# Kernel tuning notes

Hardware: AMD Instinct MI355X
Metric: run time of the kernel (lower is better)

Reference implementation:

```python
import jax, jax.numpy as jnp
import numpy as np

K = 3; PAD = 1; CIN = 64; COUT = 64; B = 4; H = 128; W = 128


def setup_inputs() -> dict:
    key = jax.random.key(0)
    k1, k2, k3 = jax.random.split(key, 3)
    x = jax.random.normal(k1, (B, CIN, H, W), dtype=jnp.float32)
    # offset-predicting conv: [2*K*K, Cin, K, K]; small init -> sub-pixel offsets
    w_off = jax.random.normal(k2, (2 * K * K, CIN, K, K), dtype=jnp.float32) * 0.01
    b_off = jnp.zeros((2 * K * K,), dtype=jnp.float32)
    # deformable conv weight (bias=False): [Cout, Cin, K, K]
    w_def = jax.random.normal(k3, (COUT, CIN, K, K), dtype=jnp.float32) * 0.05
    return {"x": x, "w_off": w_off, "b_off": b_off, "w_def": w_def}


def _deform_conv(x, w_off, b_off, w_def):
    Bb, Cin, Hh, Ww = x.shape
    KK = K * K
    # 1) predict offsets with a regular 3x3 conv (stride 1, pad 1)
    off = jax.lax.conv_general_dilated(
        x, w_off, window_strides=(1, 1), padding=[(PAD, PAD), (PAD, PAD)],
        dimension_numbers=("NCHW", "OIHW", "NCHW"))
    off = off + b_off[None, :, None, None]          # [B, 2*KK, H, W]
    off = off.reshape(Bb, KK, 2, Hh, Ww)            # torchvision layout: (dy, dx) per tap
    dy, dx = off[:, :, 0], off[:, :, 1]             # [B, KK, H, W]

    # 2) sampling coordinates: p = p0 + p_k + offset
    ky = (jnp.arange(KK) // K).astype(x.dtype)
    kx = (jnp.arange(KK) % K).astype(x.dtype)
    hh = jnp.arange(Hh, dtype=x.dtype)
    ww = jnp.arange(Ww, dtype=x.dtype)
    py = hh[None, None, :, None] - PAD + ky[None, :, None, None] + dy   # [B,KK,H,W]
    px = ww[None, None, None, :] - PAD + kx[None, :, None, None] + dx

    # 3) bilinear sampling with zero padding outside the image
    y0f = jnp.floor(py); x0f = jnp.floor(px)
    fy = py - y0f; fx = px - x0f
    y0 = y0f.astype(jnp.int32); x0 = x0f.astype(jnp.int32)
    x_flat = x.reshape(Bb, Cin, Hh * Ww)

    def gather(yi, xi):
        valid = (yi >= 0) & (yi < Hh) & (xi >= 0) & (xi < Ww)
        idx = jnp.clip(yi, 0, Hh - 1) * Ww + jnp.clip(xi, 0, Ww - 1)     # [B,KK,H,W]
        g = jax.vmap(lambda xf, ix: xf[:, ix.reshape(-1)])(x_flat, idx)  # [B,Cin,KK*H*W]
        return g.reshape(Bb, Cin, KK, Hh, Ww) * valid[:, None].astype(x.dtype)

    sampled = (gather(y0, x0)         * ((1 - fy) * (1 - fx))[:, None]
             + gather(y0, x0 + 1)     * ((1 - fy) * fx)[:, None]
             + gather(y0 + 1, x0)     * (fy * (1 - fx))[:, None]
             + gather(y0 + 1, x0 + 1) * (fy * fx)[:, None])               # [B,Cin,KK,H,W]

    # 4) convolution accumulation over (Cin, kernel taps)
    return jnp.einsum('bckhw,ock->bohw', sampled, w_def.reshape(COUT, Cin, KK))


def reference(x, w_off, b_off, w_def):
    return _deform_conv(x, w_off, b_off, w_def)
```

## Files before the change

### kernel.cpp

```cpp
#include <hip/hip_runtime.h>
#include <hip/hip_fp16.h>

#define Bn   4
#define CINc 64
#define COUTc 64
#define Hn   128
#define Wn   128
#define HW   (Hn * Wn)
#define KKc  9
#define NOFF 18

typedef short bf16x8 __attribute__((ext_vector_type(8)));
typedef float f32x4  __attribute__((ext_vector_type(4)));

__device__ inline unsigned short f2bf(float f) {
    unsigned int u = __float_as_uint(f);
    return (unsigned short)((u + 0x7fffu + ((u >> 16) & 1u)) >> 16);
}

__device__ inline void dma16(const void* g, void* l) {
#if __has_builtin(__builtin_amdgcn_global_load_lds)
    __builtin_amdgcn_global_load_lds(
        (__attribute__((address_space(1))) void*)(g),
        (__attribute__((address_space(3))) void*)(l), 16, 0, 0);
#else
    *(uint4*)l = *(const uint4*)g;
#endif
}

__global__ __launch_bounds__(256) void prep_all(
        const float* __restrict__ x, unsigned short* __restrict__ xt,
        const float* __restrict__ w_off, const float* __restrict__ w_def,
        unsigned short* __restrict__ wkb_sw, unsigned short* __restrict__ wob_sw) {
    int gb = blockIdx.x;
    int t  = threadIdx.x;
    if (gb < 1024) {
        __shared__ float s[64][65];
        int half = gb & 1;
        int h    = (gb >> 1) & 127;
        int b    = gb >> 8;
        int w0   = half * 64;
        int w = t & 63, cg = t >> 6;

        const float* xb = x + (size_t)b * CINc * HW + (size_t)h * Wn + w0 + w;
        #pragma unroll
        for (int i = 0; i < 16; ++i) {
            int c = cg * 16 + i;
            s[c][w] = xb[(size_t)c * HW];
        }
        __syncthreads();

        int cpair = t & 31, pxg = t >> 5;
        unsigned* xtp = (unsigned*)xt;
        #pragma unroll
        for (int i = 0; i < 8; ++i) {
            int px = pxg * 8 + i;
            float v0 = s[cpair * 2][px], v1 = s[cpair * 2 + 1][px];
            unsigned d = (unsigned)f2bf(v0) | ((unsigned)f2bf(v1) << 16);
            xtp[(((size_t)(b * Hn + h) * Wn) + w0 + px) * 32 + cpair] = d;
        }
        return;
    }
    int idx = (gb - 1024) * 256 + t;
    if (idx < 36864) {
        int j = idx & 7, l = (idx >> 3) & 63, s = idx >> 9;
        int k = s >> 3, kc = (s >> 2) & 1, ot = s & 3;
        int l15 = l & 15, quad = l >> 4;
        int o = ot * 16 + l15, c = kc * 32 + quad * 8 + j;
        wkb_sw[idx] = f2bf(w_def[((size_t)o * 64 + c) * 9 + k]);
    }
    int i2 = idx - 36864;
    if (i2 >= 0 && i2 < 18432) {
        int j = i2 & 7, l = (i2 >> 3) & 63, s = i2 >> 9;
        int tt = s >> 2, kc = (s >> 1) & 1, mt = s & 1;
        int l15 = l & 15, quad = l >> 4;
        int m = mt * 16 + l15, c = kc * 32 + quad * 8 + j;
        unsigned short v = 0;
        if (m < NOFF) v = f2bf(w_off[((size_t)m * 64 + c) * 9 + tt]);
        wob_sw[i2] = v;
    }
}

__global__ __launch_bounds__(256, 2) void fused_deform_v9(
        const unsigned short* __restrict__ xt,
        const unsigned short* __restrict__ wob_sw,
        const unsigned short* __restrict__ wkb_sw,
        const float* __restrict__ b_off, float* __restrict__ out) {
    __shared__ bf16x8   s_w[72 * 64];
    __shared__ unsigned s_ad[KKc][64];
    __shared__ __half2  s_wh[KKc][64][2];

    int gid  = blockIdx.x;
    int xcd  = gid & 7;
    int j    = gid >> 3;
    int half = j & 1;
    int hh   = (j >> 1) & 15;
    int b    = (j >> 5) & 3;
    int h    = xcd * 16 + hh;
    int w0   = half * 64;
    int tid  = threadIdx.x;
    int lane = tid & 63;
    int wave = __builtin_amdgcn_readfirstlane(tid >> 6);
    int l15  = lane & 15;
    int quad = lane >> 4;
    int px_blk = wave * 16 + l15;
    int p    = w0 + px_blk;

    {
        int wbase = wave * 64;
        #pragma unroll
        for (int i = 0; i < 9; ++i) {
            int ebase = i * 256 + wbase;
            dma16((const uint4*)wob_sw + ebase + lane,
                  (char*)s_w + (size_t)ebase * 16);
        }
    }

    uint4 L[9][2];
    unsigned msk[9];
    const unsigned short* xtb = xt + (size_t)b * HW * 64;
    #pragma unroll
    for (int t9 = 0; t9 < 9; ++t9) {
        int ty = t9 / 3, tx = t9 % 3;
        int y  = h - 1 + ty;
        int xg = p - 1 + tx;
        bool v = (y >= 0) && (y < Hn) && (xg >= 0) && (xg < Wn);
        msk[t9] = v ? 0xFFFFFFFFu : 0u;
        int yc = min(max(y, 0), Hn - 1);
        int xc = min(max(xg, 0), Wn - 1);
        size_t base = ((size_t)yc * Wn + xc) * 64;
        L[t9][0] = *(const uint4*)(xtb + base + quad * 8);
        L[t9][1] = *(const uint4*)(xtb + base + 32 + quad * 8);
    }
    __syncthreads();

    f32x4 oa0 = (f32x4){0.f, 0.f, 0.f, 0.f};
    f32x4 oa1 = (f32x4){0.f, 0.f, 0.f, 0.f};
    #pragma unroll
    for (int t9 = 0; t9 < 9; ++t9) {
        unsigned m = msk[t9];
        #pragma unroll
        for (int kc = 0; kc < 2; ++kc) {
            union { bf16x8 v; uint4 u; } bf;
            bf.u = L[t9][kc];
            bf.u.x &= m; bf.u.y &= m; bf.u.z &= m; bf.u.w &= m;
            bf16x8 a0 = s_w[((t9 * 2 + kc) * 2 + 0) * 64 + lane];
            bf16x8 a1 = s_w[((t9 * 2 + kc) * 2 + 1) * 64 + lane];
            oa0 = __builtin_amdgcn_mfma_f32_16x16x32_bf16(a0, bf.v, oa0, 0, 0, 0);
            oa1 = __builtin_amdgcn_mfma_f32_16x16x32_bf16(a1, bf.v, oa1, 0, 0, 0);
        }
    }

    auto phase1 = [&](int k, float dy, float dx) {
        float py  = (float)(h - 1 + k / 3) + dy;
        float pxf = (float)(p - 1 + k % 3) + dx;
        float y0f = floorf(py), x0f = floorf(pxf);
        float fy = py - y0f, fx = pxf - x0f;
        int y0 = (int)y0f, x0 = (int)x0f;
        bool vy0 = (y0 >= 0) & (y0 < Hn);
        bool vy1 = (y0 + 1 >= 0) & (y0 + 1 < Hn);
        bool vx0 = (x0 >= 0) & (x0 < Wn);
        bool vx1 = (x0 + 1 >= 0) & (x0 + 1 < Wn);
        float wy0 = vy0 ? 1.f - fy : 0.f;
        float wy1 = vy1 ? fy : 0.f;
        float wx0 = vx0 ? 1.f - fx : 0.f;
        float wx1 = vx1 ? fx : 0.f;
        int xc = min(max(x0, 0), Wn - 2);
        bool sel0 = (min(max(x0, 0), Wn - 1) != xc);
        bool sel1 = ((min(max(x0 + 1, 0), Wn - 1) - xc) == 1);
        float Wa = (sel0 ? 0.f : wx0) + (sel1 ? 0.f : wx1);
        float Wb = (sel0 ? wx0 : 0.f) + (sel1 ? wx1 : 0.f);
        int yc0 = min(max(y0, 0), Hn - 1), yc1 = min(max(y0 + 1, 0), Hn - 1);
        s_ad[k][px_blk] = (unsigned)yc0 | ((unsigned)yc1 << 8) | ((unsigned)xc << 16);
        s_wh[k][px_blk][0] = __floats2half2_rn(wy0 * Wa, wy0 * Wb);
        s_wh[k][px_blk][1] = __floats2half2_rn(wy1 * Wa, wy1 * Wb);
    };
    int kb = quad * 2;
    phase1(kb,     oa0[0] + b_off[4 * quad],     oa0[1] + b_off[4 * quad + 1]);
    phase1(kb + 1, oa0[2] + b_off[4 * quad + 2], oa0[3] + b_off[4 * quad + 3]);
    if (quad == 0)
        phase1(8, oa1[0] + b_off[16], oa1[1] + b_off[17]);
    __syncthreads();

    {
        int wbase = wave * 64;
        #pragma unroll
        for (int i = 0; i < 18; ++i) {
            int ebase = i * 256 + wbase;
            dma16((const uint4*)wkb_sw + ebase + lane,
                  (char*)s_w + (size_t)ebase * 16);
        }
    }
    __syncthreads();

    unsigned at[KKc], ab[KKc];
    float Wf[KKc][4];
    #pragma unroll
    for (int k = 0; k < KKc; ++k) {
        unsigned ad = s_ad[k][px_blk];
        int xc = (int)(ad >> 16);
        at[k] = (unsigned)(((ad & 255u) * Wn + xc) * 64);
        ab[k] = (unsigned)((((ad >> 8) & 255u) * Wn + xc) * 64);
        __half2 w01 = s_wh[k][px_blk][0], w23 = s_wh[k][px_blk][1];
        Wf[k][0] = __low2float(w01); Wf[k][1] = __high2float(w01);
        Wf[k][2] = __low2float(w23); Wf[k][3] = __high2float(w23);
    }

    f32x4 acc[4];
    #pragma unroll
    for (int ot = 0; ot < 4; ++ot) acc[ot] = (f32x4){0.f, 0.f, 0.f, 0.f};

    uint4 R[2][8];
    int co0 = quad * 8, co1 = 32 + quad * 8;

    #define FETCH(kk, st)                                            \
        do {                                                         \
            R[st][0] = *(const uint4*)(xtb + at[kk] + co0);          \
            R[st][1] = *(const uint4*)(xtb + at[kk] + 64 + co0);     \
            R[st][2] = *(const uint4*)(xtb + ab[kk] + co0);          \
            R[st][3] = *(const uint4*)(xtb + ab[kk] + 64 + co0);     \
            R[st][4] = *(const uint4*)(xtb + at[kk] + co1);          \
            R[st][5] = *(const uint4*)(xtb + at[kk] + 64 + co1);     \
            R[st][6] = *(const uint4*)(xtb + ab[kk] + co1);          \
            R[st][7] = *(const uint4*)(xtb + ab[kk] + 64 + co1);     \
        } while (0)

    FETCH(0, 0);
    #pragma unroll
    for (int k = 0; k < KKc; ++k) {
        if (k < KKc - 1) FETCH(k + 1, (k + 1) & 1);
        const uint4* C = R[k & 1];
        float W0 = Wf[k][0], W1 = Wf[k][1], W2 = Wf[k][2], W3 = Wf[k][3];
        #pragma unroll
        for (int kc = 0; kc < 2; ++kc) {
            const unsigned* t0 = (const unsigned*)&C[kc * 4 + 0];
            const unsigned* t1 = (const unsigned*)&C[kc * 4 + 1];
            const unsigned* b0 = (const unsigned*)&C[kc * 4 + 2];
            const unsigned* b1 = (const unsigned*)&C[kc * 4 + 3];
            union { bf16x8 v; unsigned u[4]; } bf;
            #pragma unroll
            for (int jd = 0; jd < 4; ++jd) {
                float t0l = __uint_as_float(t0[jd] << 16);
                float t0h = __uint_as_float(t0[jd] & 0xFFFF0000u);
                float t1l = __uint_as_float(t1[jd] << 16);
                float t1h = __uint_as_float(t1[jd] & 0xFFFF0000u);
                float b0l = __uint_as_float(b0[jd] << 16);
                float b0h = __uint_as_float(b0[jd] & 0xFFFF0000u);
                float b1l = __uint_as_float(b1[jd] << 16);
                float b1h = __uint_as_float(b1[jd] & 0xFFFF0000u);
                float vl = W0 * t0l + W1 * t1l + W2 * b0l + W3 * b1l;
                float vh = W0 * t0h + W1 * t1h + W2 * b0h + W3 * b1h;
                bf.u[jd] = (unsigned)f2bf(vl) | ((unsigned)f2bf(vh) << 16);
            }
            #pragma unroll
            for (int ot = 0; ot < 4; ++ot) {
                bf16x8 af = s_w[((k * 2 + kc) * 4 + ot) * 64 + lane];
                acc[ot] = __builtin_amdgcn_mfma_f32_16x16x32_bf16(af, bf.v, acc[ot], 0, 0, 0);
            }
        }
    }
    #undef FETCH

    #pragma unroll
    for (int ot = 0; ot < 4; ++ot)
        #pragma unroll
        for (int r = 0; r < 4; ++r) {
            int o = ot * 16 + quad * 4 + r;
            out[(((size_t)b * COUTc + o) * Hn + h) * Wn + p] = acc[ot][r];
        }
}

extern "C" void kernel_launch(void* const* d_in, const int* in_sizes, int n_in,
                              void* d_out, int out_size, void* d_ws, size_t ws_size,
                              hipStream_t stream) {
    const float* x     = (const float*)d_in[0];
    const float* w_off = (const float*)d_in[1];
    const float* b_off = (const float*)d_in[2];
    const float* w_def = (const float*)d_in[3];
    float* out = (float*)d_out;

    char* ws = (char*)d_ws;
    unsigned short* xt = (unsigned short*)ws;
    ws += (size_t)Bn * HW * CINc * sizeof(unsigned short);
    unsigned short* wkb_sw = (unsigned short*)ws;
    ws += 36864 * sizeof(unsigned short);
    unsigned short* wob_sw = (unsigned short*)ws;

    prep_all<<<1024 + 216, 256, 0, stream>>>(x, xt, w_off, w_def, wkb_sw, wob_sw);
    fused_deform_v9<<<Bn * Hn * (Wn / 64), 256, 0, stream>>>(xt, wob_sw, wkb_sw, b_off, out);
}
```

Baseline: 118.3 us.

## Process full image rows per 512-thread block and pass sampling params via shuffles

Each block now covers a whole 128-pixel row with 8 waves instead of half a row with 4, so the shared weight tiles are loaded once per row and the block count halves. Per-pixel sampling addresses and bilinear weights no longer go through shared memory; they are exchanged within the wave using shuffles, which removes the s_ad/s_wh arrays and one barrier. The weight DMA is now overlapped with the shuffle work before a single barrier. Risks include lower occupancy from the larger block and the (512,4) launch bound squeezing registers, plus fewer blocks to fill the GPU.

```diff
diff --git a/kernel.cpp b/kernel.cpp
--- a/kernel.cpp
+++ b/kernel.cpp
@@ -81,36 +81,31 @@
     }
 }
 
-__global__ __launch_bounds__(256, 2) void fused_deform_v9(
+__global__ __launch_bounds__(512, 4) void fused_deform_v10(
         const unsigned short* __restrict__ xt,
         const unsigned short* __restrict__ wob_sw,
         const unsigned short* __restrict__ wkb_sw,
         const float* __restrict__ b_off, float* __restrict__ out) {
-    __shared__ bf16x8   s_w[72 * 64];
-    __shared__ unsigned s_ad[KKc][64];
-    __shared__ __half2  s_wh[KKc][64][2];
+    __shared__ bf16x8 s_w[72 * 64];
 
     int gid  = blockIdx.x;
     int xcd  = gid & 7;
     int j    = gid >> 3;
-    int half = j & 1;
-    int hh   = (j >> 1) & 15;
-    int b    = (j >> 5) & 3;
+    int hh   = j & 15;
+    int b    = j >> 4;
     int h    = xcd * 16 + hh;
-    int w0   = half * 64;
     int tid  = threadIdx.x;
     int lane = tid & 63;
     int wave = __builtin_amdgcn_readfirstlane(tid >> 6);
     int l15  = lane & 15;
     int quad = lane >> 4;
-    int px_blk = wave * 16 + l15;
-    int p    = w0 + px_blk;
-
-    {
-        int wbase = wave * 64;
-        #pragma unroll
-        for (int i = 0; i < 9; ++i) {
-            int ebase = i * 256 + wbase;
+    int p    = wave * 16 + l15;
+
+    #pragma unroll
+    for (int i = 0; i < 5; ++i) {
+        int seg = i * 8 + wave;
+        if (seg < 36) {
+            int ebase = seg * 64;
             dma16((const uint4*)wob_sw + ebase + lane,
                   (char*)s_w + (size_t)ebase * 16);
         }
@@ -151,7 +146,10 @@
         }
     }
 
-    auto phase1 = [&](int k, float dy, float dx) {
+    unsigned my_ad[3]  = {0, 0, 0};
+    unsigned my_w01[3] = {0, 0, 0};
+    unsigned my_w23[3] = {0, 0, 0};
+    auto phase1 = [&](int k, float dy, float dx, int slot) {
         float py  = (float)(h - 1 + k / 3) + dy;
         float pxf = (float)(p - 1 + k % 3) + dx;
         float y0f = floorf(py), x0f = floorf(pxf);
@@ -171,40 +169,46 @@
         float Wa = (sel0 ? 0.f : wx0) + (sel1 ? 0.f : wx1);
         float Wb = (sel0 ? wx0 : 0.f) + (sel1 ? wx1 : 0.f);
         int yc0 = min(max(y0, 0), Hn - 1), yc1 = min(max(y0 + 1, 0), Hn - 1);
-        s_ad[k][px_blk] = (unsigned)yc0 | ((unsigned)yc1 << 8) | ((unsigned)xc << 16);
-        s_wh[k][px_blk][0] = __floats2half2_rn(wy0 * Wa, wy0 * Wb);
-        s_wh[k][px_blk][1] = __floats2half2_rn(wy1 * Wa, wy1 * Wb);
+        union { __half2 hv; unsigned u; } c01, c23;
+        c01.hv = __floats2half2_rn(wy0 * Wa, wy0 * Wb);
+        c23.hv = __floats2half2_rn(wy1 * Wa, wy1 * Wb);
+        my_ad[slot]  = (unsigned)yc0 | ((unsigned)yc1 << 8) | ((unsigned)xc << 16);
+        my_w01[slot] = c01.u;
+        my_w23[slot] = c23.u;
     };
     int kb = quad * 2;
-    phase1(kb,     oa0[0] + b_off[4 * quad],     oa0[1] + b_off[4 * quad + 1]);
-    phase1(kb + 1, oa0[2] + b_off[4 * quad + 2], oa0[3] + b_off[4 * quad + 3]);
+    phase1(kb,     oa0[0] + b_off[4 * quad],     oa0[1] + b_off[4 * quad + 1], 0);
+    phase1(kb + 1, oa0[2] + b_off[4 * quad + 2], oa0[3] + b_off[4 * quad + 3], 1);
     if (quad == 0)
-        phase1(8, oa1[0] + b_off[16], oa1[1] + b_off[17]);
+        phase1(8, oa1[0] + b_off[16], oa1[1] + b_off[17], 2);
     __syncthreads();
 
-    {
-        int wbase = wave * 64;
-        #pragma unroll
-        for (int i = 0; i < 18; ++i) {
-            int ebase = i * 256 + wbase;
-            dma16((const uint4*)wkb_sw + ebase + lane,
-                  (char*)s_w + (size_t)ebase * 16);
-        }
-    }
-    __syncthreads();
+    #pragma unroll
+    for (int i = 0; i < 9; ++i) {
+        int seg = i * 8 + wave;
+        int ebase = seg * 64;
+        dma16((const uint4*)wkb_sw + ebase + lane,
+              (char*)s_w + (size_t)ebase * 16);
+    }
 
     unsigned at[KKc], ab[KKc];
     float Wf[KKc][4];
     #pragma unroll
     for (int k = 0; k < KKc; ++k) {
-        unsigned ad = s_ad[k][px_blk];
+        int src  = (k < 8) ? ((k >> 1) * 16 + l15) : l15;
+        int slot = (k < 8) ? (k & 1) : 2;
+        unsigned ad  = (unsigned)__shfl((int)my_ad[slot],  src, 64);
+        unsigned w01 = (unsigned)__shfl((int)my_w01[slot], src, 64);
+        unsigned w23 = (unsigned)__shfl((int)my_w23[slot], src, 64);
         int xc = (int)(ad >> 16);
         at[k] = (unsigned)(((ad & 255u) * Wn + xc) * 64);
         ab[k] = (unsigned)((((ad >> 8) & 255u) * Wn + xc) * 64);
-        __half2 w01 = s_wh[k][px_blk][0], w23 = s_wh[k][px_blk][1];
-        Wf[k][0] = __low2float(w01); Wf[k][1] = __high2float(w01);
-        Wf[k][2] = __low2float(w23); Wf[k][3] = __high2float(w23);
-    }
+        union { unsigned u; __half2 hv; } c01, c23;
+        c01.u = w01; c23.u = w23;
+        Wf[k][0] = __low2float(c01.hv); Wf[k][1] = __high2float(c01.hv);
+        Wf[k][2] = __low2float(c23.hv); Wf[k][3] = __high2float(c23.hv);
+    }
+    __syncthreads();
 
     f32x4 acc[4];
     #pragma unroll
@@ -287,5 +291,5 @@
     unsigned short* wob_sw = (unsigned short*)ws;
 
     prep_all<<<1024 + 216, 256, 0, stream>>>(x, xt, w_off, w_def, wkb_sw, wob_sw);
-    fused_deform_v9<<<Bn * Hn * (Wn / 64), 256, 0, stream>>>(xt, wob_sw, wkb_sw, b_off, out);
-}
+    fused_deform_v10<<<Bn * Hn, 512, 0, stream>>>(xt, wob_sw, wkb_sw, b_off, out);
+}
```

Measured after the change: 115.4 us. -2.5%, faster.
